# Kernel tuning notes

Measured on AMD Instinct MI355X. Metric: run time of the kernel, lower is better.

Reference implementation:

```python
import jax, jax.numpy as jnp
import numpy as np

EMB = 1024
HEADS = 8
EXP = 4
EPS = 1e-5


def setup_inputs() -> dict:
    key = jax.random.key(0)
    ks = jax.random.split(key, 12)
    s = 0.02
    return {
        "x": jax.random.normal(ks[0], (4, 2048, EMB), dtype=jnp.float32),
        "wqkv_w": jax.random.normal(ks[1], (EMB, 3 * EMB), dtype=jnp.float32) * s,
        "wqkv_b": jnp.zeros((3 * EMB,), dtype=jnp.float32),
        "proj_w": jax.random.normal(ks[2], (EMB, EMB), dtype=jnp.float32) * s,
        "proj_b": jnp.zeros((EMB,), dtype=jnp.float32),
        "lin1_w": jax.random.normal(ks[3], (EMB, EXP * EMB), dtype=jnp.float32) * s,
        "lin1_b": jnp.zeros((EXP * EMB,), dtype=jnp.float32),
        "lin2_w": jax.random.normal(ks[4], (EXP * EMB, EMB), dtype=jnp.float32) * s,
        "lin2_b": jnp.zeros((EMB,), dtype=jnp.float32),
        "ln_g": jnp.ones((EMB,), dtype=jnp.float32),
        "ln_b": jnp.zeros((EMB,), dtype=jnp.float32),
    }


def _layernorm(x, g, b):
    mu = jnp.mean(x, axis=-1, keepdims=True)
    var = jnp.var(x, axis=-1, keepdims=True)
    return (x - mu) * jax.lax.rsqrt(var + EPS) * g + b


def reference(x, wqkv_w, wqkv_b, proj_w, proj_b, lin1_w, lin1_b, lin2_w, lin2_b, ln_g, ln_b):
    b, n, e = x.shape
    h = HEADS
    d = e // h
    # fused QKV; source splits '(h d w)' with w=3 innermost (interleaved)
    w = x @ wqkv_w + wqkv_b                      # [b, n, 3e]
    w = w.reshape(b, n, h, d, 3)
    w = jnp.transpose(w, (4, 0, 2, 1, 3))        # [3, b, h, n, d]
    q, k, v = w[0], w[1], w[2]
    scores = jnp.einsum('bhqd,bhkd->bhqk', q, k)  # unscaled logits (as in source)
    attn = jax.nn.softmax(scores, axis=-1) / jnp.sqrt(jnp.float32(e))
    o = jnp.einsum('bhqk,bhkd->bhqd', attn, v)
    o = jnp.transpose(o, (0, 2, 1, 3)).reshape(b, n, e)
    mha = o @ proj_w + proj_b
    x = _layernorm(x + mha, ln_g, ln_b)
    ff = (jax.nn.gelu(x @ lin1_w + lin1_b, approximate=False)) @ lin2_w + lin2_b
    return _layernorm(x + ff, ln_g, ln_b)
```

## Files before the change

### kernel.cpp

```cpp
#include <hip/hip_runtime.h>
#include <hip/hip_bf16.h>
#include <math.h>

#define B_DIM 4
#define SEQ   2048
#define EMB   1024
#define HEADS 8
#define DHEAD 128
#define M_TOK (B_DIM * SEQ)
#define FFDIM (4 * EMB)

typedef unsigned short u16;
typedef __attribute__((ext_vector_type(8))) short short8v;
typedef __attribute__((ext_vector_type(4))) float float4v;
typedef __attribute__((ext_vector_type(16))) float float16v;

__device__ __forceinline__ u16 f2b(float f) {
  union { float f; unsigned u; } a; a.f = f;
  unsigned u = a.u;
  u += 0x7fffu + ((u >> 16) & 1u);
  return (u16)(u >> 16);
}

__device__ __forceinline__ u16 f2b_hw(float f) {
  __hip_bfloat16 h = __float2bfloat16(f);
  return *(u16*)&h;
}

__device__ __forceinline__ void gload16(const void* g, void* l) {
  __builtin_amdgcn_global_load_lds(
      (const __attribute__((address_space(1))) unsigned int*)g,
      (__attribute__((address_space(3))) unsigned int*)l, 16, 0, 0);
}

__device__ __forceinline__ float gelu_inl(float v) {
  const float y = 0.7978845608028654f * (v + 0.044715f * v * v * v);
  const float e = __expf(2.0f * y);
  const float th = 1.0f - 2.0f / (e + 1.0f);
  return 0.5f * v * (1.0f + th);
}

__device__ __forceinline__ void tcvt_body(const float* __restrict__ W,
    u16* __restrict__ Wt, int K, int N, int bx, int by, int tx, int ty,
    float (*t)[33]) {
  const int n0 = bx * 32, k0 = by * 32;
  for (int j = ty; j < 32; j += 8)
    t[j][tx] = W[(size_t)(k0 + j) * N + n0 + tx];
  __syncthreads();
  for (int j = ty; j < 32; j += 8)
    Wt[(size_t)(n0 + j) * K + k0 + tx] = f2b(t[tx][j]);
}

__global__ __launch_bounds__(256) void k_prep(
    const float* __restrict__ x, const float* __restrict__ wqkv_w,
    const float* __restrict__ proj_w, const float* __restrict__ lin1_w,
    const float* __restrict__ lin2_w, u16* __restrict__ xb,
    u16* __restrict__ wqkv_t, u16* __restrict__ proj_t,
    u16* __restrict__ lin1_t, u16* __restrict__ lin2_t) {
  __shared__ float t[32][33];
  const int bid = blockIdx.x, tid = threadIdx.x;
  if (bid < 8192) {
    const int i = bid * 256 + tid;
    const float4 v = ((const float4*)x)[i];
    unsigned long long pk = (unsigned long long)f2b(v.x)
        | ((unsigned long long)f2b(v.y) << 16)
        | ((unsigned long long)f2b(v.z) << 32)
        | ((unsigned long long)f2b(v.w) << 48);
    ((unsigned long long*)xb)[i] = pk;
    return;
  }
  const int tx = tid & 31, ty = tid >> 5;
  if (bid < 11264)
    tcvt_body(wqkv_w, wqkv_t, 1024, 3072, (bid - 8192) % 96, (bid - 8192) / 96, tx, ty, t);
  else if (bid < 12288)
    tcvt_body(proj_w, proj_t, 1024, 1024, (bid - 11264) % 32, (bid - 11264) / 32, tx, ty, t);
  else if (bid < 16384)
    tcvt_body(lin1_w, lin1_t, 1024, 4096, (bid - 12288) % 128, (bid - 12288) / 128, tx, ty, t);
  else
    tcvt_body(lin2_w, lin2_t, 4096, 1024, (bid - 16384) % 32, (bid - 16384) / 32, tx, ty, t);
}

template <int EPI>
__global__ __launch_bounds__(256, 2) void k_gemm(
    const u16* __restrict__ A, const u16* __restrict__ Bt,
    const float* __restrict__ bias, const float* __restrict__ res,
    void* __restrict__ out0, int M, int N, int K) {
  __shared__ __align__(16) u16 lds[2][2][128][32];
  const int tid = threadIdx.x;
  const int l = tid & 63, w = tid >> 6;
  const int g = l >> 4, lm = l & 15;
  const int wm = w >> 1, wn = w & 1;

  const int NBX = N >> 7;
  const int nwg = NBX * (M >> 7);
  const int wg = blockIdx.x;
  const int swz = (wg & 7) * (nwg >> 3) + (wg >> 3);
  const int tn = swz % NBX, tm = swz / NBX;

  const size_t arow0 = (size_t)tm * 128;
  const size_t brow0 = (size_t)tn * 128;
  const int srow = l >> 2;
  const int scol = (l & 3) * 8;

  float4v acc[4][4];
  const float4v vzero = {0.f, 0.f, 0.f, 0.f};
#pragma unroll
  for (int i = 0; i < 4; ++i)
#pragma unroll
    for (int j = 0; j < 4; ++j) acc[i][j] = vzero;

  const int nt = K / 32;
  auto stage = [&](int t, int buf) {
    const int k0 = t * 32;
#pragma unroll
    for (int i = 0; i < 2; ++i) {
      const int r = w * 32 + i * 16 + srow;
      gload16(A + (arow0 + r) * (size_t)K + k0 + scol, &lds[buf][0][w * 32 + i * 16][0]);
      gload16(Bt + (brow0 + r) * (size_t)K + k0 + scol, &lds[buf][1][w * 32 + i * 16][0]);
    }
  };

  stage(0, 0);
  __syncthreads();
  for (int t = 0; t < nt; ++t) {
    const int buf = t & 1;
    if (t + 1 < nt) stage(t + 1, buf ^ 1);
    short8v af[4], bf[4];
#pragma unroll
    for (int mf = 0; mf < 4; ++mf)
      af[mf] = *(const short8v*)&lds[buf][0][wm * 64 + mf * 16 + lm][g * 8];
#pragma unroll
    for (int nf = 0; nf < 4; ++nf)
      bf[nf] = *(const short8v*)&lds[buf][1][wn * 64 + nf * 16 + lm][g * 8];
#pragma unroll
    for (int mf = 0; mf < 4; ++mf)
#pragma unroll
      for (int nf = 0; nf < 4; ++nf)
        acc[mf][nf] = __builtin_amdgcn_mfma_f32_16x16x32_bf16(af[mf], bf[nf], acc[mf][nf], 0, 0, 0);
    __syncthreads();
  }

#pragma unroll
  for (int mf = 0; mf < 4; ++mf)
#pragma unroll
    for (int nf = 0; nf < 4; ++nf)
#pragma unroll
      for (int r = 0; r < 4; ++r) {
        const int row = tm * 128 + wm * 64 + mf * 16 + 4 * g + r;
        const int col = tn * 128 + wn * 64 + nf * 16 + lm;
        float v = acc[mf][nf][r] + bias[col];
        if constexpr (EPI == 0) {
          const int hh = col / 384;
          const int rem = col - hh * 384;
          const int d = rem / 3;
          const int wv = rem - d * 3;
          const int btok = row >> 11, ntok = row & 2047;
          u16* dst = (u16*)out0 + (size_t)wv * ((size_t)M_TOK * EMB)
                   + (((size_t)(btok * HEADS + hh) * SEQ + ntok) * DHEAD + d);
          *dst = f2b(v);
        } else if constexpr (EPI == 2) {
          ((u16*)out0)[(size_t)row * N + col] = f2b(gelu_inl(v));
        } else {
          const size_t idx = (size_t)row * N + col;
          ((float*)out0)[idx] = v + res[idx];
        }
      }
}

__global__ __launch_bounds__(512, 2) void k_attn(
    const u16* __restrict__ q, const u16* __restrict__ k,
    const u16* __restrict__ v, u16* __restrict__ o) {
  __shared__ __align__(16) u16 KT[2][64 * 128];
  __shared__ __align__(16) u16 VT[2][64 * 128];
  const int tid = threadIdx.x;
  const int l = tid & 63, w = tid >> 6;
  const int q32 = l & 31, hi = l >> 5;
  const int i = blockIdx.x;
  const int xcd = i & 7, j = i >> 3;
  const int bh = xcd * 4 + (j >> 3);
  const int qt = j & 7;
  const int hh = bh & 7, bb = bh >> 3;
  const size_t base = (size_t)(bb * HEADS + hh) * SEQ * DHEAD;
  const int qrow0 = qt * 256 + w * 32;

  short8v qf[8];
#pragma unroll
  for (int c = 0; c < 8; ++c)
    qf[c] = *(const short8v*)(q + base + (size_t)(qrow0 + q32) * DHEAD + c * 16 + hi * 8);

  float m = -1e30f, Sden = 0.f;
  float16v O[4];
#pragma unroll
  for (int nf = 0; nf < 4; ++nf)
#pragma unroll
    for (int r = 0; r < 16; ++r) O[nf][r] = 0.f;

  const int krow = tid >> 4;
  const int kseg = (tid & 15) * 16;
  const int vp = tid & 31, vdg = tid >> 5;

  short8v va, vb2;
  auto loadV = [&](int t) {
    const u16* s0p = v + base + ((size_t)t * 64 + 2 * vp) * DHEAD + vdg * 8;
    va  = *(const short8v*)s0p;
    vb2 = *(const short8v*)(s0p + DHEAD);
  };
  auto writeV = [&](int b) {
    const int d0 = vdg * 8;
#pragma unroll
    for (int jj = 0; jj < 8; ++jj) {
      const unsigned pk = ((unsigned)(u16)va[jj]) | (((unsigned)(u16)vb2[jj]) << 16);
      const int byte = ((d0 + jj) * 128 + 4 * vp) ^ (((d0 + jj) & 7) << 4);
      *(unsigned*)((char*)&VT[b][0] + byte) = pk;
    }
  };
  auto stageK = [&](int t, int b) {
    const size_t kvbase = base + (size_t)t * 64 * DHEAD;
#pragma unroll
    for (int s = 0; s < 2; ++s) {
      const int r = s * 32 + krow;
      const int csrc = kseg ^ ((r & 7) << 4);
      gload16(k + kvbase + (size_t)r * DHEAD + (csrc >> 1),
              (u16*)&KT[b][0] + s * 4096 + tid * 8);
    }
  };

  loadV(0);
  stageK(0, 0);
  writeV(0);
  __syncthreads();

  for (int t = 0; t < 32; ++t) {
    const int buf = t & 1;
    const char* KTb = (const char*)&KT[buf][0];
    const char* VTb = (const char*)&VT[buf][0];
    if (t + 1 < 32) { loadV(t + 1); stageK(t + 1, buf ^ 1); }

    float16v S0, S1;
#pragma unroll
    for (int r = 0; r < 16; ++r) { S0[r] = 0.f; S1[r] = 0.f; }
    __builtin_amdgcn_s_setprio(1);
#pragma unroll
    for (int c = 0; c < 8; ++c) {
      const int cb = (c * 32 + hi * 16) ^ ((q32 & 7) << 4);
      const short8v kf0 = *(const short8v*)(KTb + q32 * 256 + cb);
      const short8v kf1 = *(const short8v*)(KTb + (32 + q32) * 256 + cb);
      S0 = __builtin_amdgcn_mfma_f32_32x32x16_bf16(kf0, qf[c], S0, 0, 0, 0);
      S1 = __builtin_amdgcn_mfma_f32_32x32x16_bf16(kf1, qf[c], S1, 0, 0, 0);
    }
    __builtin_amdgcn_s_setprio(0);

    float pm = -1e30f;
#pragma unroll
    for (int r = 0; r < 16; ++r) pm = fmaxf(pm, fmaxf(S0[r], S1[r]));
    pm = fmaxf(pm, __shfl_xor(pm, 32));
    if (!__all(pm <= m + 8.0f)) {
      const float nm = fmaxf(m, pm);
      const float rsc = __expf(m - nm);
      m = nm;
      Sden *= rsc;
#pragma unroll
      for (int r = 0; r < 16; ++r) {
        const float rr_ = __shfl(rsc, (r & 3) + 8 * (r >> 2) + 4 * hi, 64);
#pragma unroll
        for (int nf = 0; nf < 4; ++nf) O[nf][r] *= rr_;
      }
    }
    float ps = 0.f;
#pragma unroll
    for (int r = 0; r < 16; ++r) { S0[r] = __expf(S0[r] - m); ps += S0[r]; }
#pragma unroll
    for (int r = 0; r < 16; ++r) { S1[r] = __expf(S1[r] - m); ps += S1[r]; }
    ps += __shfl_xor(ps, 32);
    Sden += ps;

    unsigned u0[8], u1[8];
#pragma unroll
    for (int jj = 0; jj < 8; ++jj) {
      u0[jj] = (unsigned)f2b_hw(S0[2 * jj]) | ((unsigned)f2b_hw(S0[2 * jj + 1]) << 16);
      u1[jj] = (unsigned)f2b_hw(S1[2 * jj]) | ((unsigned)f2b_hw(S1[2 * jj + 1]) << 16);
    }

#pragma unroll
    for (int ks = 0; ks < 4; ++ks) {
      const int k1 = ks & 1;
      unsigned b0v, b1v, b2v, b3v;
      if (ks < 2) { b0v = u0[4 * k1]; b1v = u0[4 * k1 + 1]; b2v = u0[4 * k1 + 2]; b3v = u0[4 * k1 + 3]; }
      else        { b0v = u1[4 * k1]; b1v = u1[4 * k1 + 1]; b2v = u1[4 * k1 + 2]; b3v = u1[4 * k1 + 3]; }
      const unsigned send0 = hi ? b0v : b2v;
      const unsigned send1 = hi ? b1v : b3v;
      const unsigned rx0 = (unsigned)__shfl_xor((int)send0, 32);
      const unsigned rx1 = (unsigned)__shfl_xor((int)send1, 32);
      union { unsigned uu[4]; short8v s8; } pu;
      pu.uu[0] = hi ? rx0 : b0v;
      pu.uu[1] = hi ? rx1 : b1v;
      pu.uu[2] = hi ? b2v : rx0;
      pu.uu[3] = hi ? b3v : rx1;
      __builtin_amdgcn_s_setprio(1);
#pragma unroll
      for (int nf = 0; nf < 4; ++nf) {
        const int dr = nf * 32 + q32;
        const int vb = (dr * 128 + ks * 32 + hi * 16) ^ ((dr & 7) << 4);
        const short8v vf = *(const short8v*)(VTb + vb);
        O[nf] = __builtin_amdgcn_mfma_f32_32x32x16_bf16(pu.s8, vf, O[nf], 0, 0, 0);
      }
      __builtin_amdgcn_s_setprio(0);
    }

    if (t + 1 < 32) writeV(buf ^ 1);
    __syncthreads();
  }

  const float si = 1.0f / (Sden * 32.0f);
#pragma unroll
  for (int r = 0; r < 16; ++r) {
    const int cr = (r & 3) + 8 * (r >> 2) + 4 * hi;
    const float sio = __shfl(si, cr, 64);
    const int tok = qrow0 + cr;
#pragma unroll
    for (int nf = 0; nf < 4; ++nf)
      o[(size_t)(bb * SEQ + tok) * EMB + hh * DHEAD + nf * 32 + q32] = f2b_hw(O[nf][r] * sio);
  }
}

template <int MODE>
__global__ __launch_bounds__(256) void k_ln(const float* __restrict__ in,
    const float* __restrict__ gw, const float* __restrict__ bw,
    float* __restrict__ outf, u16* __restrict__ outb) {
  __shared__ float ps[4], pq[4];
  const int row = blockIdx.x;
  const int t = threadIdx.x;
  const float4 v = ((const float4*)(in + (size_t)row * EMB))[t];
  float s = v.x + v.y + v.z + v.w;
  float sq = v.x * v.x + v.y * v.y + v.z * v.z + v.w * v.w;
#pragma unroll
  for (int d = 1; d < 64; d <<= 1) { s += __shfl_xor(s, d); sq += __shfl_xor(sq, d); }
  const int l = t & 63, w = t >> 6;
  if (l == 0) { ps[w] = s; pq[w] = sq; }
  __syncthreads();
  s = ps[0] + ps[1] + ps[2] + ps[3];
  sq = pq[0] + pq[1] + pq[2] + pq[3];
  const float mean = s * (1.0f / 1024.0f);
  const float var = sq * (1.0f / 1024.0f) - mean * mean;
  const float rs = rsqrtf(var + 1e-5f);
  const float4 gv = ((const float4*)gw)[t];
  const float4 bv = ((const float4*)bw)[t];
  float4 ov;
  ov.x = (v.x - mean) * rs * gv.x + bv.x;
  ov.y = (v.y - mean) * rs * gv.y + bv.y;
  ov.z = (v.z - mean) * rs * gv.z + bv.z;
  ov.w = (v.w - mean) * rs * gv.w + bv.w;
  ((float4*)(outf + (size_t)row * EMB))[t] = ov;
  if constexpr (MODE == 0) {
    unsigned long long pk = (unsigned long long)f2b(ov.x)
        | ((unsigned long long)f2b(ov.y) << 16)
        | ((unsigned long long)f2b(ov.z) << 32)
        | ((unsigned long long)f2b(ov.w) << 48);
    ((unsigned long long*)(outb + (size_t)row * EMB))[t] = pk;
  }
}

extern "C" void kernel_launch(void* const* d_in, const int* in_sizes, int n_in,
                              void* d_out, int out_size, void* d_ws, size_t ws_size,
                              hipStream_t stream) {
  const float* x      = (const float*)d_in[0];
  const float* wqkv_w = (const float*)d_in[1];
  const float* wqkv_b = (const float*)d_in[2];
  const float* proj_w = (const float*)d_in[3];
  const float* proj_b = (const float*)d_in[4];
  const float* lin1_w = (const float*)d_in[5];
  const float* lin1_b = (const float*)d_in[6];
  const float* lin2_w = (const float*)d_in[7];
  const float* lin2_b = (const float*)d_in[8];
  const float* ln_g   = (const float*)d_in[9];
  const float* ln_b   = (const float*)d_in[10];

  char* ws = (char*)d_ws;
  u16*   wqkv_t = (u16*)(ws + 0);
  u16*   proj_t = (u16*)(ws + 6291456);
  u16*   lin1_t = (u16*)(ws + 8388608);
  u16*   lin2_t = (u16*)(ws + 16777216);
  u16*   qbuf   = (u16*)(ws + 25165824);
  u16*   kbuf   = (u16*)(ws + 25165824 + 16777216);
  u16*   vbuf   = (u16*)(ws + 25165824 + 33554432);
  u16*   xb     = (u16*)(ws + 75497472);
  u16*   attn_o = (u16*)(ws + 75497472);
  float* res1   = (float*)(ws + 92274688);
  u16*   hbuf   = (u16*)(ws + 92274688);
  float* x1f    = (float*)(ws + 25165824);
  u16*   x1b    = (u16*)(ws + 58720256);
  float* outf   = (float*)d_out;

  k_prep<<<20480, 256, 0, stream>>>(x, wqkv_w, proj_w, lin1_w, lin2_w,
                                    xb, wqkv_t, proj_t, lin1_t, lin2_t);

  k_gemm<0><<<(3 * EMB / 128) * (M_TOK / 128), 256, 0, stream>>>(
      xb, wqkv_t, wqkv_b, nullptr, (void*)qbuf, M_TOK, 3 * EMB, EMB);
  k_attn<<<256, 512, 0, stream>>>(qbuf, kbuf, vbuf, attn_o);
  k_gemm<1><<<(EMB / 128) * (M_TOK / 128), 256, 0, stream>>>(
      attn_o, proj_t, proj_b, x, (void*)res1, M_TOK, EMB, EMB);
  k_ln<0><<<M_TOK, 256, 0, stream>>>(res1, ln_g, ln_b, x1f, x1b);
  k_gemm<2><<<(FFDIM / 128) * (M_TOK / 128), 256, 0, stream>>>(
      x1b, lin1_t, lin1_b, nullptr, (void*)hbuf, M_TOK, FFDIM, EMB);
  k_gemm<3><<<(EMB / 128) * (M_TOK / 128), 256, 0, stream>>>(
      hbuf, lin2_t, lin2_b, x1f, (void*)outf, M_TOK, EMB, FFDIM);
  k_ln<1><<<M_TOK, 256, 0, stream>>>(outf, ln_g, ln_b, outf, nullptr);
}
```

Measured before the change: 455.1 us.

## Split attention KV range in halves and merge partial outputs

Each attention block now takes a 128-row query tile and only one half of the key/value sequence, using 32-key tiles and 256-thread blocks. This quadruples the grid from 256 to 1024 blocks and allows more blocks per CU. Unnormalised partial outputs (bf16) and per-row max and denominator are written to workspace, and a new merge kernel combines the two halves with log-sum-exp weights and writes the final head-interleaved layout. The cost is an extra kernel launch, about 32MB of extra partial traffic, and bf16 rounding of the partial outputs before the merge.

```diff
diff --git a/kernel.cpp b/kernel.cpp
--- a/kernel.cpp
+++ b/kernel.cpp
@@ -25,6 +25,10 @@
 __device__ __forceinline__ u16 f2b_hw(float f) {
   __hip_bfloat16 h = __float2bfloat16(f);
   return *(u16*)&h;
+}
+
+__device__ __forceinline__ float b2f(u16 u) {
+  union { unsigned u; float f; } x; x.u = ((unsigned)u) << 16; return x.f;
 }
 
 __device__ __forceinline__ void gload16(const void* g, void* l) {
@@ -167,21 +171,25 @@
       }
 }
 
-__global__ __launch_bounds__(512, 2) void k_attn(
+__global__ __launch_bounds__(256, 4) void k_attn(
     const u16* __restrict__ q, const u16* __restrict__ k,
-    const u16* __restrict__ v, u16* __restrict__ o) {
-  __shared__ __align__(16) u16 KT[2][64 * 128];
-  __shared__ __align__(16) u16 VT[2][64 * 128];
+    const u16* __restrict__ v, u16* __restrict__ opart,
+    float2* __restrict__ ml) {
+  __shared__ __align__(16) u16 KT[2][32 * 128];
+  __shared__ __align__(16) u16 VT[2][32 * 128];
   const int tid = threadIdx.x;
   const int l = tid & 63, w = tid >> 6;
   const int q32 = l & 31, hi = l >> 5;
   const int i = blockIdx.x;
   const int xcd = i & 7, j = i >> 3;
-  const int bh = xcd * 4 + (j >> 3);
-  const int qt = j & 7;
+  const int bh = xcd * 4 + (j >> 5);
+  const int rem = j & 31;
+  const int qt = rem >> 1;
+  const int half = rem & 1;
   const int hh = bh & 7, bb = bh >> 3;
   const size_t base = (size_t)(bb * HEADS + hh) * SEQ * DHEAD;
-  const int qrow0 = qt * 256 + w * 32;
+  const size_t khalf = base + (size_t)half * 1024 * DHEAD;
+  const int qrow0 = qt * 128 + w * 32;
 
   short8v qf[8];
 #pragma unroll
@@ -197,31 +205,31 @@
 
   const int krow = tid >> 4;
   const int kseg = (tid & 15) * 16;
-  const int vp = tid & 31, vdg = tid >> 5;
-
-  short8v va, vb2;
+  const int vp = tid & 15, vdg = tid >> 4;
+
+  short8v va, vb;
   auto loadV = [&](int t) {
-    const u16* s0p = v + base + ((size_t)t * 64 + 2 * vp) * DHEAD + vdg * 8;
-    va  = *(const short8v*)s0p;
-    vb2 = *(const short8v*)(s0p + DHEAD);
+    const u16* s0p = v + khalf + ((size_t)t * 32 + 2 * vp) * DHEAD + vdg * 8;
+    va = *(const short8v*)s0p;
+    vb = *(const short8v*)(s0p + DHEAD);
   };
   auto writeV = [&](int b) {
-    const int d0 = vdg * 8;
 #pragma unroll
     for (int jj = 0; jj < 8; ++jj) {
-      const unsigned pk = ((unsigned)(u16)va[jj]) | (((unsigned)(u16)vb2[jj]) << 16);
-      const int byte = ((d0 + jj) * 128 + 4 * vp) ^ (((d0 + jj) & 7) << 4);
+      const int d = vdg * 8 + jj;
+      const unsigned pk = ((unsigned)(u16)va[jj]) | (((unsigned)(u16)vb[jj]) << 16);
+      const int byte = d * 64 + ((4 * vp) ^ ((d & 3) << 4));
       *(unsigned*)((char*)&VT[b][0] + byte) = pk;
     }
   };
   auto stageK = [&](int t, int b) {
-    const size_t kvbase = base + (size_t)t * 64 * DHEAD;
+    const size_t kvbase = khalf + (size_t)t * 32 * DHEAD;
 #pragma unroll
     for (int s = 0; s < 2; ++s) {
-      const int r = s * 32 + krow;
+      const int r = s * 16 + krow;
       const int csrc = kseg ^ ((r & 7) << 4);
       gload16(k + kvbase + (size_t)r * DHEAD + (csrc >> 1),
-              (u16*)&KT[b][0] + s * 4096 + tid * 8);
+              (u16*)&KT[b][0] + s * 2048 + tid * 8);
     }
   };
 
@@ -236,23 +244,21 @@
     const char* VTb = (const char*)&VT[buf][0];
     if (t + 1 < 32) { loadV(t + 1); stageK(t + 1, buf ^ 1); }
 
-    float16v S0, S1;
-#pragma unroll
-    for (int r = 0; r < 16; ++r) { S0[r] = 0.f; S1[r] = 0.f; }
+    float16v S0;
+#pragma unroll
+    for (int r = 0; r < 16; ++r) S0[r] = 0.f;
     __builtin_amdgcn_s_setprio(1);
 #pragma unroll
     for (int c = 0; c < 8; ++c) {
       const int cb = (c * 32 + hi * 16) ^ ((q32 & 7) << 4);
       const short8v kf0 = *(const short8v*)(KTb + q32 * 256 + cb);
-      const short8v kf1 = *(const short8v*)(KTb + (32 + q32) * 256 + cb);
       S0 = __builtin_amdgcn_mfma_f32_32x32x16_bf16(kf0, qf[c], S0, 0, 0, 0);
-      S1 = __builtin_amdgcn_mfma_f32_32x32x16_bf16(kf1, qf[c], S1, 0, 0, 0);
     }
     __builtin_amdgcn_s_setprio(0);
 
     float pm = -1e30f;
 #pragma unroll
-    for (int r = 0; r < 16; ++r) pm = fmaxf(pm, fmaxf(S0[r], S1[r]));
+    for (int r = 0; r < 16; ++r) pm = fmaxf(pm, S0[r]);
     pm = fmaxf(pm, __shfl_xor(pm, 32));
     if (!__all(pm <= m + 8.0f)) {
       const float nm = fmaxf(m, pm);
@@ -269,24 +275,18 @@
     float ps = 0.f;
 #pragma unroll
     for (int r = 0; r < 16; ++r) { S0[r] = __expf(S0[r] - m); ps += S0[r]; }
-#pragma unroll
-    for (int r = 0; r < 16; ++r) { S1[r] = __expf(S1[r] - m); ps += S1[r]; }
     ps += __shfl_xor(ps, 32);
     Sden += ps;
 
-    unsigned u0[8], u1[8];
-#pragma unroll
-    for (int jj = 0; jj < 8; ++jj) {
+    unsigned u0[8];
+#pragma unroll
+    for (int jj = 0; jj < 8; ++jj)
       u0[jj] = (unsigned)f2b_hw(S0[2 * jj]) | ((unsigned)f2b_hw(S0[2 * jj + 1]) << 16);
-      u1[jj] = (unsigned)f2b_hw(S1[2 * jj]) | ((unsigned)f2b_hw(S1[2 * jj + 1]) << 16);
-    }
-
-#pragma unroll
-    for (int ks = 0; ks < 4; ++ks) {
-      const int k1 = ks & 1;
-      unsigned b0v, b1v, b2v, b3v;
-      if (ks < 2) { b0v = u0[4 * k1]; b1v = u0[4 * k1 + 1]; b2v = u0[4 * k1 + 2]; b3v = u0[4 * k1 + 3]; }
-      else        { b0v = u1[4 * k1]; b1v = u1[4 * k1 + 1]; b2v = u1[4 * k1 + 2]; b3v = u1[4 * k1 + 3]; }
+
+#pragma unroll
+    for (int ks = 0; ks < 2; ++ks) {
+      const unsigned b0v = u0[4 * ks], b1v = u0[4 * ks + 1];
+      const unsigned b2v = u0[4 * ks + 2], b3v = u0[4 * ks + 3];
       const unsigned send0 = hi ? b0v : b2v;
       const unsigned send1 = hi ? b1v : b3v;
       const unsigned rx0 = (unsigned)__shfl_xor((int)send0, 32);
@@ -300,8 +300,8 @@
 #pragma unroll
       for (int nf = 0; nf < 4; ++nf) {
         const int dr = nf * 32 + q32;
-        const int vb = (dr * 128 + ks * 32 + hi * 16) ^ ((dr & 7) << 4);
-        const short8v vf = *(const short8v*)(VTb + vb);
+        const int vbyte = dr * 64 + ((ks * 32 + hi * 16) ^ ((dr & 3) << 4));
+        const short8v vf = *(const short8v*)(VTb + vbyte);
         O[nf] = __builtin_amdgcn_mfma_f32_32x32x16_bf16(pu.s8, vf, O[nf], 0, 0, 0);
       }
       __builtin_amdgcn_s_setprio(0);
@@ -311,16 +311,39 @@
     __syncthreads();
   }
 
-  const float si = 1.0f / (Sden * 32.0f);
+  const size_t orow = (size_t)half * 65536 + (size_t)(bb * 8 + hh) * 2048;
 #pragma unroll
   for (int r = 0; r < 16; ++r) {
     const int cr = (r & 3) + 8 * (r >> 2) + 4 * hi;
-    const float sio = __shfl(si, cr, 64);
     const int tok = qrow0 + cr;
+    u16* dst = opart + (orow + tok) * 128;
 #pragma unroll
     for (int nf = 0; nf < 4; ++nf)
-      o[(size_t)(bb * SEQ + tok) * EMB + hh * DHEAD + nf * 32 + q32] = f2b_hw(O[nf][r] * sio);
+      dst[nf * 32 + q32] = f2b_hw(O[nf][r]);
   }
+  if (hi == 0)
+    ml[orow + qrow0 + q32] = make_float2(m, Sden);
+}
+
+__global__ __launch_bounds__(256) void k_mrg(const u16* __restrict__ opart,
+    const float2* __restrict__ ml, u16* __restrict__ o) {
+  const int idx = blockIdx.x * 256 + threadIdx.x;
+  const int row = idx >> 5;
+  const int d0 = (idx & 31) * 4;
+  const float2 ml1 = ml[row];
+  const float2 ml2 = ml[65536 + row];
+  const float mm = fmaxf(ml1.x, ml2.x);
+  const float w1 = __expf(ml1.x - mm), w2 = __expf(ml2.x - mm);
+  const float inv = 1.0f / ((w1 * ml1.y + w2 * ml2.y) * 32.0f);
+  const ushort4 a = *(const ushort4*)(opart + (size_t)row * 128 + d0);
+  const ushort4 b = *(const ushort4*)(opart + ((size_t)65536 + row) * 128 + d0);
+  ushort4 rr;
+  rr.x = f2b_hw((w1 * b2f(a.x) + w2 * b2f(b.x)) * inv);
+  rr.y = f2b_hw((w1 * b2f(a.y) + w2 * b2f(b.y)) * inv);
+  rr.z = f2b_hw((w1 * b2f(a.z) + w2 * b2f(b.z)) * inv);
+  rr.w = f2b_hw((w1 * b2f(a.w) + w2 * b2f(b.w)) * inv);
+  const int bb = row >> 14, hh = (row >> 11) & 7, tok = row & 2047;
+  *(ushort4*)(o + ((size_t)(bb * 2048 + tok)) * 1024 + hh * 128 + d0) = rr;
 }
 
 template <int MODE>
@@ -387,6 +410,8 @@
   u16*   attn_o = (u16*)(ws + 75497472);
   float* res1   = (float*)(ws + 92274688);
   u16*   hbuf   = (u16*)(ws + 92274688);
+  u16*   opart  = (u16*)(ws + 92274688);
+  float2* mlprt = (float2*)(ws + 0);
   float* x1f    = (float*)(ws + 25165824);
   u16*   x1b    = (u16*)(ws + 58720256);
   float* outf   = (float*)d_out;
@@ -396,7 +421,8 @@
 
   k_gemm<0><<<(3 * EMB / 128) * (M_TOK / 128), 256, 0, stream>>>(
       xb, wqkv_t, wqkv_b, nullptr, (void*)qbuf, M_TOK, 3 * EMB, EMB);
-  k_attn<<<256, 512, 0, stream>>>(qbuf, kbuf, vbuf, attn_o);
+  k_attn<<<1024, 256, 0, stream>>>(qbuf, kbuf, vbuf, opart, mlprt);
+  k_mrg<<<8192, 256, 0, stream>>>(opart, mlprt, attn_o);
   k_gemm<1><<<(EMB / 128) * (M_TOK / 128), 256, 0, stream>>>(
       attn_o, proj_t, proj_b, x, (void*)res1, M_TOK, EMB, EMB);
   k_ln<0><<<M_TOK, 256, 0, stream>>>(res1, ln_g, ln_b, x1f, x1b);
```

After: 563.5 us. +23.8%, slower.
